# Performance work log

Measured on AMD Instinct MI355X. Metric: run time of the kernel, lower is better.

The kernel has to match this reference:

```python
import math
import jax, jax.numpy as jnp
import numpy as np

B, N, L, D = 4, 16, 1024, 64  # batch, heads, seq len (L1=L2), head dim


def rel_shift(x):
    """Transformer-XL positional shift: [b,n,q,p]->[b,n,q,k] aligning relative positions."""
    b, n, q, k = x.shape
    x = jnp.pad(x, ((0, 0), (0, 0), (0, 0), (1, 0)))  # pad one zero column in front
    x = x.reshape(b, n, k + 1, q)
    return x[:, :, 1:, :].reshape(b, n, q, k)


def setup_inputs() -> dict:
    rng = jax.random.key(0)
    k1, k2, k3, k4, k5 = jax.random.split(rng, 5)
    query_content_biased = jax.random.normal(k1, (B, N, L, D), dtype=jnp.float32)
    query_pos_biased = jax.random.normal(k2, (B, N, L, D), dtype=jnp.float32)
    key = jax.random.normal(k3, (B, N, L, D), dtype=jnp.float32)
    value = jax.random.normal(k4, (B, N, L, D), dtype=jnp.float32)
    pos_encodings = jax.random.normal(k5, (N, L, D), dtype=jnp.float32)
    # causal mask: True = masked (as in torch masked_fill), broadcast over b,n
    mask = jnp.triu(jnp.ones((L, L), dtype=bool), k=1)[None, None]
    return {
        "query_content_biased": query_content_biased,
        "query_pos_biased": query_pos_biased,
        "key": key,
        "value": value,
        "pos_encodings": pos_encodings,
        "mask": mask,
    }


def reference(query_content_biased, query_pos_biased, key, value, pos_encodings, mask):
    # content scores: [b,n,i,j]
    weight = jnp.einsum('bnid,bnjd->bnij', query_content_biased, key)
    # positional scores, shifted into key axis
    pos_scores = jnp.einsum('bnid,npd->bnip', query_pos_biased, pos_encodings)
    weight = weight + rel_shift(pos_scores)
    weight = weight / math.sqrt(key.shape[-1])
    neg = jnp.finfo(weight.dtype).min
    weight = jnp.where(mask, neg, weight)
    weight = jax.nn.softmax(weight, axis=-1)
    weight = jnp.where(mask, jnp.zeros((), weight.dtype), weight)
    # dropout is identity at p=0.0 (eval)
    out = jnp.einsum('bnij,bnjd->bnid', weight, value)
    return (out, weight)
```

## Files before the change

### kernel.cpp

```cpp
#include <hip/hip_runtime.h>
#include <math.h>


#define Bq 4
#define Nh 16
#define Lq 1024
#define Dh 64
#define TQ 16
#define NT 512
#define LPAD 1028

typedef __attribute__((ext_vector_type(8))) short bf16x8;
typedef __attribute__((ext_vector_type(4))) float f32x4;

__device__ __forceinline__ unsigned short f2bf(float f) {
    union { float f; unsigned int u; } v; v.f = f;
    unsigned int u = v.u;
    unsigned int r = u + 0x7FFFu + ((u >> 16) & 1u);
    return (unsigned short)(r >> 16);
}

__device__ __forceinline__ bf16x8 pack8(float4 a, float4 b) {
    bf16x8 o;
    o[0] = (short)f2bf(a.x); o[1] = (short)f2bf(a.y);
    o[2] = (short)f2bf(a.z); o[3] = (short)f2bf(a.w);
    o[4] = (short)f2bf(b.x); o[5] = (short)f2bf(b.y);
    o[6] = (short)f2bf(b.z); o[7] = (short)f2bf(b.w);
    return o;
}

__device__ __forceinline__ bf16x8 ldg8(const unsigned short* p) {
    return *(const bf16x8*)p;
}

__device__ __forceinline__ float wave_max(float v) {
    #pragma unroll
    for (int o = 32; o > 0; o >>= 1) v = fmaxf(v, __shfl_xor(v, o));
    return v;
}
__device__ __forceinline__ float wave_sum(float v) {
    #pragma unroll
    for (int o = 32; o > 0; o >>= 1) v += __shfl_xor(v, o);
    return v;
}

__global__ __launch_bounds__(256) void cvt_kp_kernel(
    const float* __restrict__ K, const float* __restrict__ P,
    unsigned short* __restrict__ Kb, unsigned short* __restrict__ Pb)
{
    int b = blockIdx.x;
    const float* src; unsigned short* dst; int idx;
    if (b < 4096) { idx = b * 256 + threadIdx.x; src = K; dst = Kb; }
    else          { idx = (b - 4096) * 256 + threadIdx.x; src = P; dst = Pb; }
    float4 v = ((const float4*)src)[idx];
    ushort4 o;
    o.x = f2bf(v.x); o.y = f2bf(v.y); o.z = f2bf(v.z); o.w = f2bf(v.w);
    ((ushort4*)dst)[idx] = o;
}

__global__ __launch_bounds__(256) void vt_kernel(
    const float* __restrict__ V, unsigned short* __restrict__ Vt)
{
    __shared__ float t[64][65];
    int bn = blockIdx.x >> 4, jt = blockIdx.x & 15;
    int tid = threadIdx.x;
    int d = tid & 63, q = tid >> 6;
    const float* vb = V + ((size_t)(bn * Lq + jt * 64)) * Dh;
    #pragma unroll
    for (int r = 0; r < 16; r++) {
        int jl = r * 4 + q;
        t[jl][d] = vb[(size_t)jl * Dh + d];
    }
    __syncthreads();
    int dd = tid >> 2, jb = (tid & 3) << 4;
    bf16x8 s0, s1;
    #pragma unroll
    for (int jj = 0; jj < 8; jj++) {
        s0[jj] = (short)f2bf(t[jb + jj][dd]);
        s1[jj] = (short)f2bf(t[jb + 8 + jj][dd]);
    }
    unsigned short* drow = Vt + (((size_t)(bn * 64 + dd)) << 10) + (jt << 6) + jb;
    *(bf16x8*)drow = s0;
    *(bf16x8*)(drow + 8) = s1;
}

__global__ __launch_bounds__(NT, 4) void relattn_kernel(
    const float* __restrict__ QC, const float* __restrict__ QP,
    const unsigned short* __restrict__ Kb, const unsigned short* __restrict__ Pb,
    const unsigned short* __restrict__ Vtb,
    float* __restrict__ out, float* __restrict__ wout)
{
    __shared__ __align__(16) float s_s[TQ][LPAD];
    __shared__ __align__(16) float dscr[4][64][4];

    const int tid  = threadIdx.x;
    const int w    = tid >> 6, lane = tid & 63;
    const int ln   = lane & 15, quad = lane >> 4;

    const int bidx = blockIdx.x;
    const int wg   = ((bidx & 7) << 9) | (bidx >> 3);
    const int bn   = wg >> 6, qt = wg & 63;
    const int nh   = bn & 15;
    const int i0   = qt << 4, i1 = i0 + 15;

    const float* qcrow = QC + (((size_t)(bn << 10) + i0 + ln) << 6) + (quad << 3);
    const float* qprow = QP + (((size_t)(bn << 10) + i0 + ln) << 6) + (quad << 3);
    bf16x8 aC0 = pack8(*(const float4*)qcrow,        *(const float4*)(qcrow + 4));
    bf16x8 aC1 = pack8(*(const float4*)(qcrow + 32), *(const float4*)(qcrow + 36));
    bf16x8 aP0 = pack8(*(const float4*)qprow,        *(const float4*)(qprow + 4));
    bf16x8 aP1 = pack8(*(const float4*)(qprow + 32), *(const float4*)(qprow + 36));

    const unsigned short* kbase = Kb + (((size_t)(bn << 10)) << 6) + (quad << 3);
    #pragma unroll
    for (int ct = 0; ct < 8; ct++) {
        int c0 = ((ct << 3) + w) << 4;
        if (c0 <= i1) {
            const unsigned short* kr = kbase + ((size_t)(c0 + ln) << 6);
            f32x4 acc = {0.f, 0.f, 0.f, 0.f};
            acc = __builtin_amdgcn_mfma_f32_16x16x32_bf16(aC0, ldg8(kr),      acc, 0, 0, 0);
            acc = __builtin_amdgcn_mfma_f32_16x16x32_bf16(aC1, ldg8(kr + 32), acc, 0, 0, 0);
            #pragma unroll
            for (int rg = 0; rg < 4; rg++)
                s_s[(quad << 2) + rg][c0 + ln] = acc[rg];
        }
    }
    __syncthreads();

    const unsigned short* pbase = Pb + (((size_t)(nh << 10)) << 6) + (quad << 3);
    #pragma unroll
    for (int ct = 0; ct < 8; ct++) {
        int p0 = ((ct << 3) + w) << 4;
        if (p0 + i0 + 30 >= 1023) {
            const unsigned short* pr = pbase + ((size_t)(p0 + ln) << 6);
            f32x4 acc = {0.f, 0.f, 0.f, 0.f};
            acc = __builtin_amdgcn_mfma_f32_16x16x32_bf16(aP0, ldg8(pr),      acc, 0, 0, 0);
            acc = __builtin_amdgcn_mfma_f32_16x16x32_bf16(aP1, ldg8(pr + 32), acc, 0, 0, 0);
            int p = p0 + ln;
            #pragma unroll
            for (int rg = 0; rg < 4; rg++) {
                int row = (quad << 2) + rg;
                int j = p + i0 + row - 1023;
                if (j >= 0) s_s[row][j] += acc[rg];
            }
        }
    }
    __syncthreads();

    #pragma unroll
    for (int rr = 0; rr < 2; rr++) {
        int r = (w << 1) + rr;
        int i = i0 + r;
        float v[16];
        #pragma unroll
        for (int c = 0; c < 4; c++) {
            float4 t = *(float4*)&s_s[r][(c << 8) + (lane << 2)];
            v[c * 4 + 0] = t.x; v[c * 4 + 1] = t.y;
            v[c * 4 + 2] = t.z; v[c * 4 + 3] = t.w;
        }
        float mx = -3.0e38f;
        #pragma unroll
        for (int c = 0; c < 4; c++) {
            int j = (c << 8) + (lane << 2);
            #pragma unroll
            for (int e = 0; e < 4; e++)
                if (j + e <= i) mx = fmaxf(mx, v[c * 4 + e]);
        }
        mx = wave_max(mx);
        float sum = 0.f;
        #pragma unroll
        for (int c = 0; c < 4; c++) {
            int j = (c << 8) + (lane << 2);
            #pragma unroll
            for (int e = 0; e < 4; e++) {
                float t = (j + e <= i) ? __expf((v[c * 4 + e] - mx) * 0.125f) : 0.f;
                sum += t;
                v[c * 4 + e] = t;
            }
        }
        sum = wave_sum(sum);
        float inv = 1.0f / sum;
        float* wrow = wout + (((size_t)(bn << 10) + i) << 10);
        char*  brow = (char*)s_s + (size_t)r * (LPAD * 4);
        #pragma unroll
        for (int c = 0; c < 4; c++) {
            int j = (c << 8) + (lane << 2);
            float4 e;
            e.x = v[c * 4 + 0] * inv; e.y = v[c * 4 + 1] * inv;
            e.z = v[c * 4 + 2] * inv; e.w = v[c * 4 + 3] * inv;
            *(float4*)&wrow[j] = e;
            ushort4 h;
            h.x = f2bf(e.x); h.y = f2bf(e.y); h.z = f2bf(e.z); h.w = f2bf(e.w);
            *(ushort4*)(brow + (size_t)j * 2) = h;
        }
    }
    __syncthreads();

    f32x4 o = {0.f, 0.f, 0.f, 0.f};
    const int n0 = (w & 3) << 4;
    const int h  = w >> 2;
    const unsigned short* vtb = Vtb + (((size_t)(bn << 6) + n0 + ln) << 10);
    const char* abase = (const char*)s_s + (size_t)ln * (LPAD * 4);
    const int ksteps = (i0 + 16 + 31) >> 5;
    for (int ks = h; ks < ksteps; ks += 2) {
        int k0 = (ks << 5) + (quad << 3);
        bf16x8 af = *(const bf16x8*)(abase + (size_t)k0 * 2);
        bf16x8 vb = ldg8(vtb + k0);
        o = __builtin_amdgcn_mfma_f32_16x16x32_bf16(af, vb, o, 0, 0, 0);
    }
    if (h == 1)
        *(f32x4*)&dscr[w & 3][lane][0] = o;
    __syncthreads();
    if (h == 0) {
        f32x4 o2 = *(f32x4*)&dscr[w][lane][0];
        o[0] += o2[0]; o[1] += o2[1]; o[2] += o2[2]; o[3] += o2[3];
        float* obase = out + (((size_t)(bn << 10) + i0) << 6);
        #pragma unroll
        for (int rg = 0; rg < 4; rg++)
            obase[((size_t)((quad << 2) + rg) << 6) + n0 + ln] = o[rg];
    }
}

extern "C" void kernel_launch(void* const* d_in, const int* in_sizes, int n_in,
                              void* d_out, int out_size, void* d_ws, size_t ws_size,
                              hipStream_t stream) {
    const float* qc = (const float*)d_in[0];
    const float* qp = (const float*)d_in[1];
    const float* K  = (const float*)d_in[2];
    const float* V  = (const float*)d_in[3];
    const float* P  = (const float*)d_in[4];

    float* out  = (float*)d_out;
    float* wout = out + (size_t)Bq * Nh * Lq * Dh;

    const size_t NQ = (size_t)Bq * Nh * Lq * Dh;
    const size_t NP = (size_t)Nh * Lq * Dh;
    unsigned short* Kb  = (unsigned short*)d_ws;
    unsigned short* Pb  = Kb + NQ;
    unsigned short* Vtb = Pb + NP;

    cvt_kp_kernel<<<4096 + 1024, 256, 0, stream>>>(K, P, Kb, Pb);
    vt_kernel<<<Bq * Nh * 16, 256, 0, stream>>>(V, Vtb);
    relattn_kernel<<<Bq * Nh * (Lq / TQ), NT, 0, stream>>>(qc, qp, Kb, Pb, Vtb, out, wout);
}
```

Measured before the change: 453.5 us.

## Switch to fp16 MFMA with half-precision score buffer and reversed tile order

Replaces the bf16 software rounding with native fp16 conversions and fp16 MFMA, and stores the score tile in LDS as fp16 instead of fp32. This halves the shared-memory footprint so launch bounds can ask for 8 blocks per CU, raising occupancy. Query tiles are also issued in reverse order so the longest causal rows start first, which should balance the load. The fp16 scores and accumulated positional terms could overflow or lose precision before softmax, which is a risk to accuracy.

```diff
diff --git a/kernel.cpp b/kernel.cpp
--- a/kernel.cpp
+++ b/kernel.cpp
@@ -8,29 +8,18 @@
 #define Dh 64
 #define TQ 16
 #define NT 512
-#define LPAD 1028
-
-typedef __attribute__((ext_vector_type(8))) short bf16x8;
+#define LROW 1032
+
+typedef _Float16 h16;
+typedef __attribute__((ext_vector_type(8))) _Float16 f16x8;
+typedef __attribute__((ext_vector_type(4))) _Float16 f16x4;
 typedef __attribute__((ext_vector_type(4))) float f32x4;
 
-__device__ __forceinline__ unsigned short f2bf(float f) {
-    union { float f; unsigned int u; } v; v.f = f;
-    unsigned int u = v.u;
-    unsigned int r = u + 0x7FFFu + ((u >> 16) & 1u);
-    return (unsigned short)(r >> 16);
-}
-
-__device__ __forceinline__ bf16x8 pack8(float4 a, float4 b) {
-    bf16x8 o;
-    o[0] = (short)f2bf(a.x); o[1] = (short)f2bf(a.y);
-    o[2] = (short)f2bf(a.z); o[3] = (short)f2bf(a.w);
-    o[4] = (short)f2bf(b.x); o[5] = (short)f2bf(b.y);
-    o[6] = (short)f2bf(b.z); o[7] = (short)f2bf(b.w);
+__device__ __forceinline__ f16x8 pack8h(float4 a, float4 b) {
+    f16x8 o;
+    o[0] = (h16)a.x; o[1] = (h16)a.y; o[2] = (h16)a.z; o[3] = (h16)a.w;
+    o[4] = (h16)b.x; o[5] = (h16)b.y; o[6] = (h16)b.z; o[7] = (h16)b.w;
     return o;
-}
-
-__device__ __forceinline__ bf16x8 ldg8(const unsigned short* p) {
-    return *(const bf16x8*)p;
 }
 
 __device__ __forceinline__ float wave_max(float v) {
@@ -46,20 +35,20 @@
 
 __global__ __launch_bounds__(256) void cvt_kp_kernel(
     const float* __restrict__ K, const float* __restrict__ P,
-    unsigned short* __restrict__ Kb, unsigned short* __restrict__ Pb)
+    h16* __restrict__ Kb, h16* __restrict__ Pb)
 {
     int b = blockIdx.x;
-    const float* src; unsigned short* dst; int idx;
+    const float* src; h16* dst; int idx;
     if (b < 4096) { idx = b * 256 + threadIdx.x; src = K; dst = Kb; }
     else          { idx = (b - 4096) * 256 + threadIdx.x; src = P; dst = Pb; }
     float4 v = ((const float4*)src)[idx];
-    ushort4 o;
-    o.x = f2bf(v.x); o.y = f2bf(v.y); o.z = f2bf(v.z); o.w = f2bf(v.w);
-    ((ushort4*)dst)[idx] = o;
+    f16x4 o;
+    o[0] = (h16)v.x; o[1] = (h16)v.y; o[2] = (h16)v.z; o[3] = (h16)v.w;
+    ((f16x4*)dst)[idx] = o;
 }
 
 __global__ __launch_bounds__(256) void vt_kernel(
-    const float* __restrict__ V, unsigned short* __restrict__ Vt)
+    const float* __restrict__ V, h16* __restrict__ Vt)
 {
     __shared__ float t[64][65];
     int bn = blockIdx.x >> 4, jt = blockIdx.x & 15;
@@ -73,24 +62,24 @@
     }
     __syncthreads();
     int dd = tid >> 2, jb = (tid & 3) << 4;
-    bf16x8 s0, s1;
+    f16x8 s0, s1;
     #pragma unroll
     for (int jj = 0; jj < 8; jj++) {
-        s0[jj] = (short)f2bf(t[jb + jj][dd]);
-        s1[jj] = (short)f2bf(t[jb + 8 + jj][dd]);
-    }
-    unsigned short* drow = Vt + (((size_t)(bn * 64 + dd)) << 10) + (jt << 6) + jb;
-    *(bf16x8*)drow = s0;
-    *(bf16x8*)(drow + 8) = s1;
-}
-
-__global__ __launch_bounds__(NT, 4) void relattn_kernel(
+        s0[jj] = (h16)t[jb + jj][dd];
+        s1[jj] = (h16)t[jb + 8 + jj][dd];
+    }
+    h16* drow = Vt + (((size_t)(bn * 64 + dd)) << 10) + (jt << 6) + jb;
+    *(f16x8*)drow = s0;
+    *(f16x8*)(drow + 8) = s1;
+}
+
+__global__ __launch_bounds__(NT, 8) void relattn_kernel(
     const float* __restrict__ QC, const float* __restrict__ QP,
-    const unsigned short* __restrict__ Kb, const unsigned short* __restrict__ Pb,
-    const unsigned short* __restrict__ Vtb,
+    const h16* __restrict__ Kb, const h16* __restrict__ Pb,
+    const h16* __restrict__ Vtb,
     float* __restrict__ out, float* __restrict__ wout)
 {
-    __shared__ __align__(16) float s_s[TQ][LPAD];
+    __shared__ __align__(16) h16 s_s[TQ][LROW];
     __shared__ __align__(16) float dscr[4][64][4];
 
     const int tid  = threadIdx.x;
@@ -99,48 +88,49 @@
 
     const int bidx = blockIdx.x;
     const int wg   = ((bidx & 7) << 9) | (bidx >> 3);
-    const int bn   = wg >> 6, qt = wg & 63;
+    const int bn   = wg >> 6, qt = 63 - (wg & 63);
     const int nh   = bn & 15;
     const int i0   = qt << 4, i1 = i0 + 15;
 
     const float* qcrow = QC + (((size_t)(bn << 10) + i0 + ln) << 6) + (quad << 3);
     const float* qprow = QP + (((size_t)(bn << 10) + i0 + ln) << 6) + (quad << 3);
-    bf16x8 aC0 = pack8(*(const float4*)qcrow,        *(const float4*)(qcrow + 4));
-    bf16x8 aC1 = pack8(*(const float4*)(qcrow + 32), *(const float4*)(qcrow + 36));
-    bf16x8 aP0 = pack8(*(const float4*)qprow,        *(const float4*)(qprow + 4));
-    bf16x8 aP1 = pack8(*(const float4*)(qprow + 32), *(const float4*)(qprow + 36));
-
-    const unsigned short* kbase = Kb + (((size_t)(bn << 10)) << 6) + (quad << 3);
+    f16x8 aC0 = pack8h(*(const float4*)qcrow,        *(const float4*)(qcrow + 4));
+    f16x8 aC1 = pack8h(*(const float4*)(qcrow + 32), *(const float4*)(qcrow + 36));
+    f16x8 aP0 = pack8h(*(const float4*)qprow,        *(const float4*)(qprow + 4));
+    f16x8 aP1 = pack8h(*(const float4*)(qprow + 32), *(const float4*)(qprow + 36));
+
+    const h16* kbase = Kb + (((size_t)(bn << 10)) << 6) + (quad << 3);
     #pragma unroll
     for (int ct = 0; ct < 8; ct++) {
         int c0 = ((ct << 3) + w) << 4;
         if (c0 <= i1) {
-            const unsigned short* kr = kbase + ((size_t)(c0 + ln) << 6);
+            const h16* kr = kbase + ((size_t)(c0 + ln) << 6);
             f32x4 acc = {0.f, 0.f, 0.f, 0.f};
-            acc = __builtin_amdgcn_mfma_f32_16x16x32_bf16(aC0, ldg8(kr),      acc, 0, 0, 0);
-            acc = __builtin_amdgcn_mfma_f32_16x16x32_bf16(aC1, ldg8(kr + 32), acc, 0, 0, 0);
+            acc = __builtin_amdgcn_mfma_f32_16x16x32_f16(aC0, *(const f16x8*)kr,        acc, 0, 0, 0);
+            acc = __builtin_amdgcn_mfma_f32_16x16x32_f16(aC1, *(const f16x8*)(kr + 32), acc, 0, 0, 0);
             #pragma unroll
             for (int rg = 0; rg < 4; rg++)
-                s_s[(quad << 2) + rg][c0 + ln] = acc[rg];
-        }
-    }
-    __syncthreads();
-
-    const unsigned short* pbase = Pb + (((size_t)(nh << 10)) << 6) + (quad << 3);
+                s_s[(quad << 2) + rg][c0 + ln] = (h16)acc[rg];
+        }
+    }
+    __syncthreads();
+
+    const h16* pbase = Pb + (((size_t)(nh << 10)) << 6) + (quad << 3);
     #pragma unroll
     for (int ct = 0; ct < 8; ct++) {
         int p0 = ((ct << 3) + w) << 4;
         if (p0 + i0 + 30 >= 1023) {
-            const unsigned short* pr = pbase + ((size_t)(p0 + ln) << 6);
+            const h16* pr = pbase + ((size_t)(p0 + ln) << 6);
             f32x4 acc = {0.f, 0.f, 0.f, 0.f};
-            acc = __builtin_amdgcn_mfma_f32_16x16x32_bf16(aP0, ldg8(pr),      acc, 0, 0, 0);
-            acc = __builtin_amdgcn_mfma_f32_16x16x32_bf16(aP1, ldg8(pr + 32), acc, 0, 0, 0);
+            acc = __builtin_amdgcn_mfma_f32_16x16x32_f16(aP0, *(const f16x8*)pr,        acc, 0, 0, 0);
+            acc = __builtin_amdgcn_mfma_f32_16x16x32_f16(aP1, *(const f16x8*)(pr + 32), acc, 0, 0, 0);
             int p = p0 + ln;
             #pragma unroll
             for (int rg = 0; rg < 4; rg++) {
                 int row = (quad << 2) + rg;
                 int j = p + i0 + row - 1023;
-                if (j >= 0) s_s[row][j] += acc[rg];
+                if (j >= 0)
+                    s_s[row][j] = (h16)((float)s_s[row][j] + acc[rg]);
             }
         }
     }
@@ -153,9 +143,9 @@
         float v[16];
         #pragma unroll
         for (int c = 0; c < 4; c++) {
-            float4 t = *(float4*)&s_s[r][(c << 8) + (lane << 2)];
-            v[c * 4 + 0] = t.x; v[c * 4 + 1] = t.y;
-            v[c * 4 + 2] = t.z; v[c * 4 + 3] = t.w;
+            f16x4 t = *(f16x4*)&s_s[r][(c << 8) + (lane << 2)];
+            v[c * 4 + 0] = (float)t[0]; v[c * 4 + 1] = (float)t[1];
+            v[c * 4 + 2] = (float)t[2]; v[c * 4 + 3] = (float)t[3];
         }
         float mx = -3.0e38f;
         #pragma unroll
@@ -180,7 +170,6 @@
         sum = wave_sum(sum);
         float inv = 1.0f / sum;
         float* wrow = wout + (((size_t)(bn << 10) + i) << 10);
-        char*  brow = (char*)s_s + (size_t)r * (LPAD * 4);
         #pragma unroll
         for (int c = 0; c < 4; c++) {
             int j = (c << 8) + (lane << 2);
@@ -188,9 +177,9 @@
             e.x = v[c * 4 + 0] * inv; e.y = v[c * 4 + 1] * inv;
             e.z = v[c * 4 + 2] * inv; e.w = v[c * 4 + 3] * inv;
             *(float4*)&wrow[j] = e;
-            ushort4 h;
-            h.x = f2bf(e.x); h.y = f2bf(e.y); h.z = f2bf(e.z); h.w = f2bf(e.w);
-            *(ushort4*)(brow + (size_t)j * 2) = h;
+            f16x4 hh;
+            hh[0] = (h16)e.x; hh[1] = (h16)e.y; hh[2] = (h16)e.z; hh[3] = (h16)e.w;
+            *(f16x4*)&s_s[r][j] = hh;
         }
     }
     __syncthreads();
@@ -198,14 +187,14 @@
     f32x4 o = {0.f, 0.f, 0.f, 0.f};
     const int n0 = (w & 3) << 4;
     const int h  = w >> 2;
-    const unsigned short* vtb = Vtb + (((size_t)(bn << 6) + n0 + ln) << 10);
-    const char* abase = (const char*)s_s + (size_t)ln * (LPAD * 4);
+    const h16* vtb = Vtb + (((size_t)(bn << 6) + n0 + ln) << 10);
+    const h16* abase = &s_s[ln][0];
     const int ksteps = (i0 + 16 + 31) >> 5;
     for (int ks = h; ks < ksteps; ks += 2) {
         int k0 = (ks << 5) + (quad << 3);
-        bf16x8 af = *(const bf16x8*)(abase + (size_t)k0 * 2);
-        bf16x8 vb = ldg8(vtb + k0);
-        o = __builtin_amdgcn_mfma_f32_16x16x32_bf16(af, vb, o, 0, 0, 0);
+        f16x8 af = *(const f16x8*)(abase + k0);
+        f16x8 vb = *(const f16x8*)(vtb + k0);
+        o = __builtin_amdgcn_mfma_f32_16x16x32_f16(af, vb, o, 0, 0, 0);
     }
     if (h == 1)
         *(f32x4*)&dscr[w & 3][lane][0] = o;
@@ -234,9 +223,9 @@
 
     const size_t NQ = (size_t)Bq * Nh * Lq * Dh;
     const size_t NP = (size_t)Nh * Lq * Dh;
-    unsigned short* Kb  = (unsigned short*)d_ws;
-    unsigned short* Pb  = Kb + NQ;
-    unsigned short* Vtb = Pb + NP;
+    h16* Kb  = (h16*)d_ws;
+    h16* Pb  = Kb + NQ;
+    h16* Vtb = Pb + NP;
 
     cvt_kp_kernel<<<4096 + 1024, 256, 0, stream>>>(K, P, Kb, Pb);
     vt_kernel<<<Bq * Nh * 16, 256, 0, stream>>>(V, Vtb);
```

Result: no change. 444.7 us (-2.0%).
